# Performance work log

Measured on AMD Instinct MI355X. Metric: run time of the kernel, lower is better.

The kernel has to match this reference:

```python
import jax, jax.numpy as jnp
import numpy as np

H = 1024           # hidden_size
E = 8              # num_experts
I = 4096 // E      # expert_intermediate_size = 512
V = 32000          # vocab_size
T = 4096           # num_tokens


def setup_inputs() -> dict:
    key = jax.random.key(0)
    ks = jax.random.split(key, 6)
    x = jax.random.normal(ks[0], (T, H), dtype=jnp.float32)
    token_ids = jax.random.randint(ks[1], (T,), 0, V, dtype=jnp.int64)
    mu = jax.random.normal(ks[2], (T, H), dtype=jnp.float32)
    # learned parameters (kaiming-like scale)
    gate_up_proj = jax.random.normal(ks[3], (E, H, 2 * I), dtype=jnp.float32) * (1.0 / np.sqrt(H))
    down_proj = jax.random.normal(ks[4], (E, I, H), dtype=jnp.float32) * (1.0 / np.sqrt(I))
    mu_w = jax.random.normal(ks[5], (E, H), dtype=jnp.float32) * 0.02  # mu_router.weight [E, H]
    return {"x": x, "token_ids": token_ids, "mu": mu,
            "gate_up_proj": gate_up_proj, "down_proj": down_proj, "mu_w": mu_w}


def reference(x, token_ids, mu, gate_up_proj, down_proj, mu_w):
    # deterministic base routing: expert = token_id % num_experts
    tid = jnp.clip(token_ids, 0, V - 1)
    base_expert = tid % E                                   # [T]
    # mu router biases the routing decision
    mu_logits = mu @ mu_w.T                                 # [T, E]
    combined = jax.nn.one_hot(base_expert, E, dtype=jnp.float32) * 10.0 + mu_logits
    expert_ids = jnp.argmax(combined, axis=-1)              # [T]

    out = jnp.zeros_like(x)
    # fixed small loop over experts; rows not routed to e are discarded by the mask,
    # so computing the dense GEMM over all tokens gives identical selected rows.
    for e in range(E):
        mask = (expert_ids == e)                            # [T]
        gu = x @ gate_up_proj[e]                            # [T, 2I]
        gate, up = gu[:, :I], gu[:, I:]
        inter = jax.nn.silu(gate) * up                      # [T, I]
        y = inter @ down_proj[e]                            # [T, H]
        out = jnp.where(mask[:, None], y, out)
    return out
```

## Files before the change

### kernel.cpp

```cpp
#include <hip/hip_runtime.h>
#include <cmath>

constexpr int T_DIM = 4096;
constexpr int H_DIM = 1024;
constexpr int E_DIM = 8;
constexpr int I_DIM = 512;
constexpr int V_DIM = 32000;

typedef _Float16 half_t;
typedef __attribute__((ext_vector_type(8))) _Float16 halfx8;
typedef __attribute__((ext_vector_type(4))) _Float16 halfx4;
typedef __attribute__((ext_vector_type(4))) float floatx4;

#define GLOAD16(g, l)                                                        \
    __builtin_amdgcn_global_load_lds(                                        \
        (const __attribute__((address_space(1))) void*)(g),                  \
        (__attribute__((address_space(3))) void*)(l), 16, 0, 0)

constexpr int  CNT_STRIDE  = 16;
constexpr size_t OFF_COUNTS = 0;
constexpr size_t OFF_EID    = 1024;
constexpr size_t OFF_TOKL   = OFF_EID + (size_t)T_DIM * 4;
constexpr size_t OFF_XB     = OFF_TOKL + (size_t)E_DIM * T_DIM * 4;
constexpr size_t OFF_GUPT   = OFF_XB + (size_t)T_DIM * H_DIM * 2;
constexpr size_t OFF_DOWNT  = OFF_GUPT + (size_t)E_DIM * 2 * I_DIM * H_DIM * 2;
constexpr size_t OFF_INTER  = OFF_DOWNT + (size_t)E_DIM * H_DIM * I_DIM * 2;

__global__ __launch_bounds__(256) void prep_kernel(
    const float* __restrict__ x, const float* __restrict__ gup,
    const float* __restrict__ mu, const int* __restrict__ token_ids,
    const float* __restrict__ mu_w, half_t* __restrict__ xb,
    half_t* __restrict__ gupT, int* __restrict__ expert_id)
{
    const int z = blockIdx.z, bx = blockIdx.x, by = blockIdx.y;
    const int tid = threadIdx.x;

    if (z >= 2) {
        const int t = ((z - 2) * 256 + by) * 8 + bx;

        const float4 m = *(const float4*)&mu[(size_t)t * H_DIM + tid * 4];
        float acc[E_DIM];
#pragma unroll
        for (int e = 0; e < E_DIM; ++e) {
            const float4 w = *(const float4*)&mu_w[e * H_DIM + tid * 4];
            acc[e] = m.x * w.x + m.y * w.y + m.z * w.z + m.w * w.w;
        }
#pragma unroll
        for (int e = 0; e < E_DIM; ++e) {
#pragma unroll
            for (int off = 32; off > 0; off >>= 1)
                acc[e] += __shfl_down(acc[e], off, 64);
        }
        __shared__ float part[4][E_DIM];
        const int lane = tid & 63, w = tid >> 6;
        if (lane == 0) {
#pragma unroll
            for (int e = 0; e < E_DIM; ++e) part[w][e] = acc[e];
        }
        __syncthreads();
        if (tid == 0) {
            int tk = token_ids[t];
            tk = min(max(tk, 0), V_DIM - 1);
            const int be = tk & (E_DIM - 1);
            float best = -1e30f; int bi = 0;
#pragma unroll
            for (int e = 0; e < E_DIM; ++e) {
                const float c = part[0][e] + part[1][e] + part[2][e] + part[3][e]
                              + (e == be ? 10.f : 0.f);
                if (c > best) { best = c; bi = e; }
            }
            expert_id[t] = bi;
        }
        return;
    }

    if (z == 1) {
        const int idx = by * 8 + bx;
        if (idx >= 512) return;
#pragma unroll
        for (int p = 0; p < 4; ++p) {
            const size_t i = (size_t)idx * 8192 + p * 2048 + tid * 8;
            const float4 v0 = *(const float4*)&x[i];
            const float4 v1 = *(const float4*)&x[i + 4];
            halfx8 h = { (half_t)v0.x, (half_t)v0.y, (half_t)v0.z, (half_t)v0.w,
                         (half_t)v1.x, (half_t)v1.y, (half_t)v1.z, (half_t)v1.w };
            *(halfx8*)&xb[i] = h;
        }
        return;
    }

    __shared__ float tile[64][65];
    const float* se = gup + (size_t)bx * H_DIM * (2 * I_DIM);
    half_t* de = gupT + (size_t)bx * (2 * I_DIM) * H_DIM;
    constexpr int N = 1024, K = H_DIM;
    const int n0 = (by & 15) * 64, k0 = (by >> 4) * 64;
    const int c4 = (tid & 15) * 4, r0 = tid >> 4;
#pragma unroll
    for (int p = 0; p < 4; ++p) {
        const int r = r0 + p * 16;
        const float4 v = *(const float4*)&se[(size_t)(k0 + r) * N + n0 + c4];
        tile[r][c4 + 0] = v.x; tile[r][c4 + 1] = v.y;
        tile[r][c4 + 2] = v.z; tile[r][c4 + 3] = v.w;
    }
    __syncthreads();
#pragma unroll
    for (int p = 0; p < 4; ++p) {
        const int n = r0 + p * 16;
        const int kc = c4;
        halfx4 h = { (half_t)tile[kc + 0][n], (half_t)tile[kc + 1][n],
                     (half_t)tile[kc + 2][n], (half_t)tile[kc + 3][n] };
        *(halfx4*)&de[(size_t)(n0 + n) * K + k0 + kc] = h;
    }
}

__global__ __launch_bounds__(1024) void scatter_kernel(
    const int* __restrict__ expert_id, int* __restrict__ counts,
    int* __restrict__ tok_list)
{
    const int e = blockIdx.x;
    const int tid = threadIdx.x;
    const int lane = tid & 63, wv = tid >> 6;
    __shared__ int wcnt[16];
    int base = 0;
#pragma unroll
    for (int r = 0; r < 4; ++r) {
        const int t = r * 1024 + tid;
        const bool m = (expert_id[t] == e);
        const unsigned long long mask = __ballot(m);
        const int wrank = (int)__popcll(mask & ((1ull << lane) - 1ull));
        if (lane == 0) wcnt[wv] = (int)__popcll(mask);
        __syncthreads();
        int pre = 0, tot = 0;
#pragma unroll
        for (int i = 0; i < 16; ++i) {
            const int c = wcnt[i];
            pre += (i < wv) ? c : 0;
            tot += c;
        }
        if (m) tok_list[e * T_DIM + base + pre + wrank] = t;
        base += tot;
        __syncthreads();
    }
    if (tid == 0) counts[e * CNT_STRIDE] = base;
}

__global__ __launch_bounds__(256) void gemm1_mfma_kernel(
    const half_t* __restrict__ xb, const half_t* __restrict__ gupT,
    const float* __restrict__ down, half_t* __restrict__ downT,
    const int* __restrict__ counts, const int* __restrict__ tok_list,
    half_t* __restrict__ inter)
{
    __shared__ __align__(16) char smraw[49152 + 64 * 4];
    const int tid = threadIdx.x;
    const int e = blockIdx.x;

    if (blockIdx.z >= 64) {
        float (*tile)[65] = (float (*)[65])smraw;
        const float* se = down + (size_t)e * I_DIM * H_DIM;
        half_t* de = downT + (size_t)e * H_DIM * I_DIM;
        const int n0 = (blockIdx.z - 64) * 64, k0 = blockIdx.y * 64;
        const int c4 = (tid & 15) * 4, r0 = tid >> 4;
#pragma unroll
        for (int p = 0; p < 4; ++p) {
            const int r = r0 + p * 16;
            const float4 v = *(const float4*)&se[(size_t)(k0 + r) * H_DIM + n0 + c4];
            tile[r][c4 + 0] = v.x; tile[r][c4 + 1] = v.y;
            tile[r][c4 + 2] = v.z; tile[r][c4 + 3] = v.w;
        }
        __syncthreads();
#pragma unroll
        for (int p = 0; p < 4; ++p) {
            const int n = r0 + p * 16;
            const int kc = c4;
            halfx4 h = { (half_t)tile[kc + 0][n], (half_t)tile[kc + 1][n],
                         (half_t)tile[kc + 2][n], (half_t)tile[kc + 3][n] };
            *(halfx4*)&de[(size_t)(n0 + n) * I_DIM + k0 + kc] = h;
        }
        return;
    }

    const int count = counts[e * CNT_STRIDE];
    const int m0 = blockIdx.z * 64;
    if (m0 >= count) return;
    const int n0 = blockIdx.y * 64;

    half_t* const As0 = (half_t*)smraw;
    half_t* const As1 = (half_t*)(smraw + 8192);
    half_t* const Bs0 = (half_t*)(smraw + 16384);
    half_t* const Bs1 = (half_t*)(smraw + 32768);
    int* const toks = (int*)(smraw + 49152);

    if (tid < 64) {
        const int m = m0 + tid;
        toks[tid] = (m < count) ? tok_list[e * T_DIM + m] : -1;
    }
    __syncthreads();

    const half_t* We = gupT + (size_t)e * (2 * I_DIM) * H_DIM;

    const int lane = tid & 63;
    const int w = tid >> 6;
    const int lr = lane >> 3, lc = lane & 7;

    const half_t* aptr[2]; const half_t* bptr[4];
    half_t *a0l[2], *a1l[2], *b0l[4], *b1l[4];
#pragma unroll
    for (int j = 0; j < 2; ++j) {
        const int r = w * 16 + j * 8 + lr;
        const int cg = lc ^ (r & 7);
        const int tk = toks[r];
        aptr[j] = xb + (size_t)(tk < 0 ? 0 : tk) * H_DIM + cg * 8;
        const int off = (w * 16 + j * 8) * 64;
        a0l[j] = As0 + off; a1l[j] = As1 + off;
    }
#pragma unroll
    for (int j = 0; j < 4; ++j) {
        const int n = w * 32 + j * 8 + lr;
        const int col = (n < 64) ? (n0 + n) : (I_DIM + n0 + (n - 64));
        const int cg = lc ^ (n & 7);
        bptr[j] = We + (size_t)col * H_DIM + cg * 8;
        const int off = (w * 32 + j * 8) * 64;
        b0l[j] = Bs0 + off; b1l[j] = Bs1 + off;
    }

    const floatx4 fzero = {0.f, 0.f, 0.f, 0.f};
    floatx4 accg[2][2], accu[2][2];
#pragma unroll
    for (int i = 0; i < 2; ++i)
#pragma unroll
        for (int j = 0; j < 2; ++j) { accg[i][j] = fzero; accu[i][j] = fzero; }

    const int wr = w >> 1, wc = w & 1;
    const int fm = lane & 15, q = lane >> 4;
    const int fm7 = fm & 7;

    auto mfma_phase = [&](const half_t* A_, const half_t* B_) {
#pragma unroll
        for (int ks = 0; ks < 2; ++ks) {
            const int swz = ((ks * 4 + q) ^ fm7) * 8;
            const halfx8 a0 = *(const halfx8*)&A_[(32 * wr + fm) * 64 + swz];
            const halfx8 a1 = *(const halfx8*)&A_[(32 * wr + 16 + fm) * 64 + swz];
#pragma unroll
            for (int ct = 0; ct < 2; ++ct) {
                const int ng = wc * 32 + ct * 16 + fm;
                const halfx8 bg = *(const halfx8*)&B_[ng * 64 + swz];
                const halfx8 bu = *(const halfx8*)&B_[(64 + ng) * 64 + swz];
                accg[0][ct] = __builtin_amdgcn_mfma_f32_16x16x32_f16(a0, bg, accg[0][ct], 0, 0, 0);
                accg[1][ct] = __builtin_amdgcn_mfma_f32_16x16x32_f16(a1, bg, accg[1][ct], 0, 0, 0);
                accu[0][ct] = __builtin_amdgcn_mfma_f32_16x16x32_f16(a0, bu, accu[0][ct], 0, 0, 0);
                accu[1][ct] = __builtin_amdgcn_mfma_f32_16x16x32_f16(a1, bu, accu[1][ct], 0, 0, 0);
            }
        }
    };

#pragma unroll
    for (int j = 0; j < 2; ++j) GLOAD16(aptr[j], a0l[j]);
#pragma unroll
    for (int j = 0; j < 4; ++j) GLOAD16(bptr[j], b0l[j]);
    __syncthreads();

    for (int it = 0; it < H_DIM / 64; it += 2) {
        const int k1 = (it + 1) * 64;
        if (k1 < H_DIM) {
#pragma unroll
            for (int j = 0; j < 2; ++j) GLOAD16(aptr[j] + k1, a1l[j]);
#pragma unroll
            for (int j = 0; j < 4; ++j) GLOAD16(bptr[j] + k1, b1l[j]);
        }
        mfma_phase(As0, Bs0);
        __syncthreads();
        const int k2 = (it + 2) * 64;
        if (k2 < H_DIM) {
#pragma unroll
            for (int j = 0; j < 2; ++j) GLOAD16(aptr[j] + k2, a0l[j]);
#pragma unroll
            for (int j = 0; j < 4; ++j) GLOAD16(bptr[j] + k2, b0l[j]);
        }
        mfma_phase(As1, Bs1);
        __syncthreads();
    }

#pragma unroll
    for (int rt = 0; rt < 2; ++rt)
#pragma unroll
        for (int r = 0; r < 4; ++r) {
            const int row = 32 * wr + 16 * rt + q * 4 + r;
            const int tk = toks[row];
            if (tk < 0) continue;
#pragma unroll
            for (int ct = 0; ct < 2; ++ct) {
                const float g = accg[rt][ct][r];
                const float u = accu[rt][ct][r];
                const float s = g / (1.f + __expf(-g)) * u;
                inter[(size_t)tk * I_DIM + n0 + wc * 32 + ct * 16 + fm] = (half_t)s;
            }
        }
}

__global__ __launch_bounds__(256) void gemm2_mfma_kernel(
    const half_t* __restrict__ inter, const half_t* __restrict__ downT,
    const int* __restrict__ counts, const int* __restrict__ tok_list,
    float* __restrict__ out)
{
    const int e = blockIdx.x;
    const int count = counts[e * CNT_STRIDE];
    const int m0 = blockIdx.z * 64;
    if (m0 >= count) return;
    const int n0 = blockIdx.y * 128;

    __shared__ __align__(16) char smraw[49152 + 64 * 4];
    half_t* const As0 = (half_t*)smraw;
    half_t* const As1 = (half_t*)(smraw + 8192);
    half_t* const Bs0 = (half_t*)(smraw + 16384);
    half_t* const Bs1 = (half_t*)(smraw + 32768);
    int* const toks = (int*)(smraw + 49152);

    const int tid = threadIdx.x;
    if (tid < 64) {
        const int m = m0 + tid;
        toks[tid] = (m < count) ? tok_list[e * T_DIM + m] : -1;
    }
    __syncthreads();

    const half_t* De = downT + (size_t)e * H_DIM * I_DIM;

    const int lane = tid & 63;
    const int w = tid >> 6;
    const int lr = lane >> 3, lc = lane & 7;

    const half_t* aptr[2]; const half_t* bptr[4];
    half_t *a0l[2], *a1l[2], *b0l[4], *b1l[4];
#pragma unroll
    for (int j = 0; j < 2; ++j) {
        const int r = w * 16 + j * 8 + lr;
        const int cg = lc ^ (r & 7);
        const int tk = toks[r];
        aptr[j] = inter + (size_t)(tk < 0 ? 0 : tk) * I_DIM + cg * 8;
        const int off = (w * 16 + j * 8) * 64;
        a0l[j] = As0 + off; a1l[j] = As1 + off;
    }
#pragma unroll
    for (int j = 0; j < 4; ++j) {
        const int n = w * 32 + j * 8 + lr;
        const int cg = lc ^ (n & 7);
        bptr[j] = De + (size_t)(n0 + n) * I_DIM + cg * 8;
        const int off = (w * 32 + j * 8) * 64;
        b0l[j] = Bs0 + off; b1l[j] = Bs1 + off;
    }

    const floatx4 fzero = {0.f, 0.f, 0.f, 0.f};
    floatx4 acc[2][4];
#pragma unroll
    for (int i = 0; i < 2; ++i)
#pragma unroll
        for (int j = 0; j < 4; ++j) acc[i][j] = fzero;

    const int wr = w >> 1, wc = w & 1;
    const int fm = lane & 15, q = lane >> 4;
    const int fm7 = fm & 7;

    auto mfma_phase = [&](const half_t* A_, const half_t* B_) {
#pragma unroll
        for (int ks = 0; ks < 2; ++ks) {
            const int swz = ((ks * 4 + q) ^ fm7) * 8;
            const halfx8 a0 = *(const halfx8*)&A_[(32 * wr + fm) * 64 + swz];
            const halfx8 a1 = *(const halfx8*)&A_[(32 * wr + 16 + fm) * 64 + swz];
#pragma unroll
            for (int ct = 0; ct < 4; ++ct) {
                const halfx8 b = *(const halfx8*)&B_[(wc * 64 + ct * 16 + fm) * 64 + swz];
                acc[0][ct] = __builtin_amdgcn_mfma_f32_16x16x32_f16(a0, b, acc[0][ct], 0, 0, 0);
                acc[1][ct] = __builtin_amdgcn_mfma_f32_16x16x32_f16(a1, b, acc[1][ct], 0, 0, 0);
            }
        }
    };

#pragma unroll
    for (int j = 0; j < 2; ++j) GLOAD16(aptr[j], a0l[j]);
#pragma unroll
    for (int j = 0; j < 4; ++j) GLOAD16(bptr[j], b0l[j]);
    __syncthreads();

    for (int it = 0; it < I_DIM / 64; it += 2) {
        const int k1 = (it + 1) * 64;
        if (k1 < I_DIM) {
#pragma unroll
            for (int j = 0; j < 2; ++j) GLOAD16(aptr[j] + k1, a1l[j]);
#pragma unroll
            for (int j = 0; j < 4; ++j) GLOAD16(bptr[j] + k1, b1l[j]);
        }
        mfma_phase(As0, Bs0);
        __syncthreads();
        const int k2 = (it + 2) * 64;
        if (k2 < I_DIM) {
#pragma unroll
            for (int j = 0; j < 2; ++j) GLOAD16(aptr[j] + k2, a0l[j]);
#pragma unroll
            for (int j = 0; j < 4; ++j) GLOAD16(bptr[j] + k2, b0l[j]);
        }
        mfma_phase(As1, Bs1);
        __syncthreads();
    }

#pragma unroll
    for (int rt = 0; rt < 2; ++rt)
#pragma unroll
        for (int r = 0; r < 4; ++r) {
            const int row = 32 * wr + 16 * rt + q * 4 + r;
            const int tk = toks[row];
            if (tk < 0) continue;
#pragma unroll
            for (int ct = 0; ct < 4; ++ct)
                out[(size_t)tk * H_DIM + n0 + wc * 64 + ct * 16 + fm] = acc[rt][ct][r];
        }
}

extern "C" void kernel_launch(void* const* d_in, const int* in_sizes, int n_in,
                              void* d_out, int out_size, void* d_ws, size_t ws_size,
                              hipStream_t stream)
{
    const float* x         = (const float*)d_in[0];
    const int*   token_ids = (const int*)  d_in[1];
    const float* mu        = (const float*)d_in[2];
    const float* gup       = (const float*)d_in[3];
    const float* down      = (const float*)d_in[4];
    const float* mu_w      = (const float*)d_in[5];
    float* out = (float*)d_out;

    char* ws = (char*)d_ws;
    int*    counts    = (int*)(ws + OFF_COUNTS);
    int*    expert_id = (int*)(ws + OFF_EID);
    int*    tok_list  = (int*)(ws + OFF_TOKL);
    half_t* xb        = (half_t*)(ws + OFF_XB);
    half_t* gupT      = (half_t*)(ws + OFF_GUPT);
    half_t* downT     = (half_t*)(ws + OFF_DOWNT);
    half_t* inter     = (half_t*)(ws + OFF_INTER);

    prep_kernel<<<dim3(8, 256, 4), 256, 0, stream>>>(
        x, gup, mu, token_ids, mu_w, xb, gupT, expert_id);
    scatter_kernel<<<E_DIM, 1024, 0, stream>>>(expert_id, counts, tok_list);
    gemm1_mfma_kernel<<<dim3(E_DIM, 8, 80), 256, 0, stream>>>(
        xb, gupT, down, downT, counts, tok_list, inter);
    gemm2_mfma_kernel<<<dim3(E_DIM, 8, T_DIM / 64), 256, 0, stream>>>(
        inter, downT, counts, tok_list, out);
}
```

Before: 156.7 us.

## Fuse all four stages into one persistent cooperative kernel with grid syncs

Replaces the four separate launches (routing prep, scatter, gemm1 plus down transpose, gemm2) with a single cooperative kernel of 512 persistent blocks. Work is distributed with grid-stride loops and separated by grid.sync barriers. This removes the launch gaps between kernels. In exchange it serialises stages that previously overlapped (routing vs weight transposes), adds grid barrier cost, and caps concurrency at 512 blocks for the GEMMs.

Result: slower. 338.9 us (+116.2%).

```diff
diff --git a/kernel.cpp b/kernel.cpp
--- a/kernel.cpp
+++ b/kernel.cpp
@@ -1,5 +1,8 @@
 #include <hip/hip_runtime.h>
+#include <hip/hip_cooperative_groups.h>
 #include <cmath>
+
+namespace cg = cooperative_groups;
 
 constexpr int T_DIM = 4096;
 constexpr int H_DIM = 1024;
@@ -26,163 +29,152 @@
 constexpr size_t OFF_DOWNT  = OFF_GUPT + (size_t)E_DIM * 2 * I_DIM * H_DIM * 2;
 constexpr size_t OFF_INTER  = OFF_DOWNT + (size_t)E_DIM * H_DIM * I_DIM * 2;
 
-__global__ __launch_bounds__(256) void prep_kernel(
+__global__ __launch_bounds__(256) void fused_kernel(
     const float* __restrict__ x, const float* __restrict__ gup,
-    const float* __restrict__ mu, const int* __restrict__ token_ids,
-    const float* __restrict__ mu_w, half_t* __restrict__ xb,
-    half_t* __restrict__ gupT, int* __restrict__ expert_id)
+    const float* __restrict__ down, const float* __restrict__ mu,
+    const int* __restrict__ token_ids, const float* __restrict__ mu_w,
+    half_t* __restrict__ xb, half_t* __restrict__ gupT,
+    half_t* __restrict__ downT, int* __restrict__ expert_id,
+    int* __restrict__ counts, int* __restrict__ tok_list,
+    half_t* __restrict__ inter, float* __restrict__ out)
 {
-    const int z = blockIdx.z, bx = blockIdx.x, by = blockIdx.y;
+    __shared__ __align__(16) char smraw[49152 + 256];
     const int tid = threadIdx.x;
-
-    if (z >= 2) {
-        const int t = ((z - 2) * 256 + by) * 8 + bx;
-
-        const float4 m = *(const float4*)&mu[(size_t)t * H_DIM + tid * 4];
-        float acc[E_DIM];
-#pragma unroll
-        for (int e = 0; e < E_DIM; ++e) {
-            const float4 w = *(const float4*)&mu_w[e * H_DIM + tid * 4];
-            acc[e] = m.x * w.x + m.y * w.y + m.z * w.z + m.w * w.w;
-        }
-#pragma unroll
-        for (int e = 0; e < E_DIM; ++e) {
-#pragma unroll
-            for (int off = 32; off > 0; off >>= 1)
-                acc[e] += __shfl_down(acc[e], off, 64);
-        }
-        __shared__ float part[4][E_DIM];
-        const int lane = tid & 63, w = tid >> 6;
-        if (lane == 0) {
-#pragma unroll
-            for (int e = 0; e < E_DIM; ++e) part[w][e] = acc[e];
-        }
-        __syncthreads();
-        if (tid == 0) {
-            int tk = token_ids[t];
-            tk = min(max(tk, 0), V_DIM - 1);
-            const int be = tk & (E_DIM - 1);
-            float best = -1e30f; int bi = 0;
+    const int bx = blockIdx.x;
+    const int NB = gridDim.x;
+    const int lane = tid & 63, wv = tid >> 6;
+    cg::grid_group grid = cg::this_grid();
+
+    {
+        float (*part)[E_DIM] = (float (*)[E_DIM])smraw;
+        for (int t = bx; t < T_DIM; t += NB) {
+            const float4 m = *(const float4*)&mu[(size_t)t * H_DIM + tid * 4];
+            float acc[E_DIM];
 #pragma unroll
             for (int e = 0; e < E_DIM; ++e) {
-                const float c = part[0][e] + part[1][e] + part[2][e] + part[3][e]
-                              + (e == be ? 10.f : 0.f);
-                if (c > best) { best = c; bi = e; }
-            }
-            expert_id[t] = bi;
-        }
-        return;
+                const float4 w = *(const float4*)&mu_w[e * H_DIM + tid * 4];
+                acc[e] = m.x * w.x + m.y * w.y + m.z * w.z + m.w * w.w;
+            }
+#pragma unroll
+            for (int e = 0; e < E_DIM; ++e) {
+#pragma unroll
+                for (int off = 32; off > 0; off >>= 1)
+                    acc[e] += __shfl_down(acc[e], off, 64);
+            }
+            if (lane == 0) {
+#pragma unroll
+                for (int e = 0; e < E_DIM; ++e) part[wv][e] = acc[e];
+            }
+            __syncthreads();
+            if (tid == 0) {
+                int tk = token_ids[t];
+                tk = min(max(tk, 0), V_DIM - 1);
+                const int be = tk & (E_DIM - 1);
+                float best = -1e30f; int bi = 0;
+#pragma unroll
+                for (int e = 0; e < E_DIM; ++e) {
+                    const float c = part[0][e] + part[1][e] + part[2][e] + part[3][e]
+                                  + (e == be ? 10.f : 0.f);
+                    if (c > best) { best = c; bi = e; }
+                }
+                expert_id[t] = bi;
+            }
+            __syncthreads();
+        }
     }
-
-    if (z == 1) {
-        const int idx = by * 8 + bx;
-        if (idx >= 512) return;
-#pragma unroll
-        for (int p = 0; p < 4; ++p) {
-            const size_t i = (size_t)idx * 8192 + p * 2048 + tid * 8;
-            const float4 v0 = *(const float4*)&x[i];
-            const float4 v1 = *(const float4*)&x[i + 4];
-            halfx8 h = { (half_t)v0.x, (half_t)v0.y, (half_t)v0.z, (half_t)v0.w,
-                         (half_t)v1.x, (half_t)v1.y, (half_t)v1.z, (half_t)v1.w };
-            *(halfx8*)&xb[i] = h;
-        }
-        return;
+    grid.sync();
+
+    {
+        constexpr int N_SC = 8, N_GT = 2048, N_CV = 512, N_DT = 1024;
+        for (int it = bx; it < N_SC + N_GT + N_CV + N_DT; it += NB) {
+            if (it < N_SC) {
+                const int e = it;
+                int* wcnt = (int*)smraw;
+                int base = 0;
+#pragma unroll 1
+                for (int r = 0; r < 16; ++r) {
+                    const int t = r * 256 + tid;
+                    const bool m = (expert_id[t] == e);
+                    const unsigned long long mask = __ballot(m);
+                    const int wrank = (int)__popcll(mask & ((1ull << lane) - 1ull));
+                    if (lane == 0) wcnt[wv] = (int)__popcll(mask);
+                    __syncthreads();
+                    int pre = 0, tot = 0;
+#pragma unroll
+                    for (int i = 0; i < 4; ++i) {
+                        const int c = wcnt[i];
+                        pre += (i < wv) ? c : 0;
+                        tot += c;
+                    }
+                    if (m) tok_list[e * T_DIM + base + pre + wrank] = t;
+                    base += tot;
+                    __syncthreads();
+                }
+                if (tid == 0) counts[e * CNT_STRIDE] = base;
+                __syncthreads();
+            } else if (it < N_SC + N_GT) {
+                const int tno = it - N_SC;
+                const int e = tno >> 8, r = tno & 255;
+                const int n0 = (r & 15) * 64, k0 = (r >> 4) * 64;
+                float (*tile)[65] = (float (*)[65])smraw;
+                const float* se = gup + (size_t)e * H_DIM * (2 * I_DIM);
+                half_t* de = gupT + (size_t)e * (2 * I_DIM) * H_DIM;
+                const int c4 = (tid & 15) * 4, r0 = tid >> 4;
+#pragma unroll
+                for (int p = 0; p < 4; ++p) {
+                    const int rr = r0 + p * 16;
+                    const float4 v = *(const float4*)&se[(size_t)(k0 + rr) * 1024 + n0 + c4];
+                    tile[rr][c4 + 0] = v.x; tile[rr][c4 + 1] = v.y;
+                    tile[rr][c4 + 2] = v.z; tile[rr][c4 + 3] = v.w;
+                }
+                __syncthreads();
+#pragma unroll
+                for (int p = 0; p < 4; ++p) {
+                    const int n = r0 + p * 16;
+                    halfx4 h = { (half_t)tile[c4 + 0][n], (half_t)tile[c4 + 1][n],
+                                 (half_t)tile[c4 + 2][n], (half_t)tile[c4 + 3][n] };
+                    *(halfx4*)&de[(size_t)(n0 + n) * H_DIM + k0 + c4] = h;
+                }
+                __syncthreads();
+            } else if (it < N_SC + N_GT + N_CV) {
+                const int idx = it - (N_SC + N_GT);
+#pragma unroll
+                for (int p = 0; p < 4; ++p) {
+                    const size_t i = (size_t)idx * 8192 + p * 2048 + tid * 8;
+                    const float4 v0 = *(const float4*)&x[i];
+                    const float4 v1 = *(const float4*)&x[i + 4];
+                    halfx8 h = { (half_t)v0.x, (half_t)v0.y, (half_t)v0.z, (half_t)v0.w,
+                                 (half_t)v1.x, (half_t)v1.y, (half_t)v1.z, (half_t)v1.w };
+                    *(halfx8*)&xb[i] = h;
+                }
+            } else {
+                const int tno = it - (N_SC + N_GT + N_CV);
+                const int e = tno >> 7, r = tno & 127;
+                const int n0 = (r & 15) * 64, k0 = (r >> 4) * 64;
+                float (*tile)[65] = (float (*)[65])smraw;
+                const float* se = down + (size_t)e * I_DIM * H_DIM;
+                half_t* de = downT + (size_t)e * H_DIM * I_DIM;
+                const int c4 = (tid & 15) * 4, r0 = tid >> 4;
+#pragma unroll
+                for (int p = 0; p < 4; ++p) {
+                    const int rr = r0 + p * 16;
+                    const float4 v = *(const float4*)&se[(size_t)(k0 + rr) * H_DIM + n0 + c4];
+                    tile[rr][c4 + 0] = v.x; tile[rr][c4 + 1] = v.y;
+                    tile[rr][c4 + 2] = v.z; tile[rr][c4 + 3] = v.w;
+                }
+                __syncthreads();
+#pragma unroll
+                for (int p = 0; p < 4; ++p) {
+                    const int n = r0 + p * 16;
+                    halfx4 h = { (half_t)tile[c4 + 0][n], (half_t)tile[c4 + 1][n],
+                                 (half_t)tile[c4 + 2][n], (half_t)tile[c4 + 3][n] };
+                    *(halfx4*)&de[(size_t)(n0 + n) * I_DIM + k0 + c4] = h;
+                }
+                __syncthreads();
+            }
+        }
     }
-
-    __shared__ float tile[64][65];
-    const float* se = gup + (size_t)bx * H_DIM * (2 * I_DIM);
-    half_t* de = gupT + (size_t)bx * (2 * I_DIM) * H_DIM;
-    constexpr int N = 1024, K = H_DIM;
-    const int n0 = (by & 15) * 64, k0 = (by >> 4) * 64;
-    const int c4 = (tid & 15) * 4, r0 = tid >> 4;
-#pragma unroll
-    for (int p = 0; p < 4; ++p) {
-        const int r = r0 + p * 16;
-        const float4 v = *(const float4*)&se[(size_t)(k0 + r) * N + n0 + c4];
-        tile[r][c4 + 0] = v.x; tile[r][c4 + 1] = v.y;
-        tile[r][c4 + 2] = v.z; tile[r][c4 + 3] = v.w;
-    }
-    __syncthreads();
-#pragma unroll
-    for (int p = 0; p < 4; ++p) {
-        const int n = r0 + p * 16;
-        const int kc = c4;
-        halfx4 h = { (half_t)tile[kc + 0][n], (half_t)tile[kc + 1][n],
-                     (half_t)tile[kc + 2][n], (half_t)tile[kc + 3][n] };
-        *(halfx4*)&de[(size_t)(n0 + n) * K + k0 + kc] = h;
-    }
-}
-
-__global__ __launch_bounds__(1024) void scatter_kernel(
-    const int* __restrict__ expert_id, int* __restrict__ counts,
-    int* __restrict__ tok_list)
-{
-    const int e = blockIdx.x;
-    const int tid = threadIdx.x;
-    const int lane = tid & 63, wv = tid >> 6;
-    __shared__ int wcnt[16];
-    int base = 0;
-#pragma unroll
-    for (int r = 0; r < 4; ++r) {
-        const int t = r * 1024 + tid;
-        const bool m = (expert_id[t] == e);
-        const unsigned long long mask = __ballot(m);
-        const int wrank = (int)__popcll(mask & ((1ull << lane) - 1ull));
-        if (lane == 0) wcnt[wv] = (int)__popcll(mask);
-        __syncthreads();
-        int pre = 0, tot = 0;
-#pragma unroll
-        for (int i = 0; i < 16; ++i) {
-            const int c = wcnt[i];
-            pre += (i < wv) ? c : 0;
-            tot += c;
-        }
-        if (m) tok_list[e * T_DIM + base + pre + wrank] = t;
-        base += tot;
-        __syncthreads();
-    }
-    if (tid == 0) counts[e * CNT_STRIDE] = base;
-}
-
-__global__ __launch_bounds__(256) void gemm1_mfma_kernel(
-    const half_t* __restrict__ xb, const half_t* __restrict__ gupT,
-    const float* __restrict__ down, half_t* __restrict__ downT,
-    const int* __restrict__ counts, const int* __restrict__ tok_list,
-    half_t* __restrict__ inter)
-{
-    __shared__ __align__(16) char smraw[49152 + 64 * 4];
-    const int tid = threadIdx.x;
-    const int e = blockIdx.x;
-
-    if (blockIdx.z >= 64) {
-        float (*tile)[65] = (float (*)[65])smraw;
-        const float* se = down + (size_t)e * I_DIM * H_DIM;
-        half_t* de = downT + (size_t)e * H_DIM * I_DIM;
-        const int n0 = (blockIdx.z - 64) * 64, k0 = blockIdx.y * 64;
-        const int c4 = (tid & 15) * 4, r0 = tid >> 4;
-#pragma unroll
-        for (int p = 0; p < 4; ++p) {
-            const int r = r0 + p * 16;
-            const float4 v = *(const float4*)&se[(size_t)(k0 + r) * H_DIM + n0 + c4];
-            tile[r][c4 + 0] = v.x; tile[r][c4 + 1] = v.y;
-            tile[r][c4 + 2] = v.z; tile[r][c4 + 3] = v.w;
-        }
-        __syncthreads();
-#pragma unroll
-        for (int p = 0; p < 4; ++p) {
-            const int n = r0 + p * 16;
-            const int kc = c4;
-            halfx4 h = { (half_t)tile[kc + 0][n], (half_t)tile[kc + 1][n],
-                         (half_t)tile[kc + 2][n], (half_t)tile[kc + 3][n] };
-            *(halfx4*)&de[(size_t)(n0 + n) * I_DIM + k0 + kc] = h;
-        }
-        return;
-    }
-
-    const int count = counts[e * CNT_STRIDE];
-    const int m0 = blockIdx.z * 64;
-    if (m0 >= count) return;
-    const int n0 = blockIdx.y * 64;
+    grid.sync();
 
     half_t* const As0 = (half_t*)smraw;
     half_t* const As1 = (half_t*)(smraw + 8192);
@@ -190,228 +182,218 @@
     half_t* const Bs1 = (half_t*)(smraw + 32768);
     int* const toks = (int*)(smraw + 49152);
 
-    if (tid < 64) {
-        const int m = m0 + tid;
-        toks[tid] = (m < count) ? tok_list[e * T_DIM + m] : -1;
-    }
-    __syncthreads();
-
-    const half_t* We = gupT + (size_t)e * (2 * I_DIM) * H_DIM;
-
-    const int lane = tid & 63;
     const int w = tid >> 6;
     const int lr = lane >> 3, lc = lane & 7;
-
-    const half_t* aptr[2]; const half_t* bptr[4];
-    half_t *a0l[2], *a1l[2], *b0l[4], *b1l[4];
-#pragma unroll
-    for (int j = 0; j < 2; ++j) {
-        const int r = w * 16 + j * 8 + lr;
-        const int cg = lc ^ (r & 7);
-        const int tk = toks[r];
-        aptr[j] = xb + (size_t)(tk < 0 ? 0 : tk) * H_DIM + cg * 8;
-        const int off = (w * 16 + j * 8) * 64;
-        a0l[j] = As0 + off; a1l[j] = As1 + off;
-    }
-#pragma unroll
-    for (int j = 0; j < 4; ++j) {
-        const int n = w * 32 + j * 8 + lr;
-        const int col = (n < 64) ? (n0 + n) : (I_DIM + n0 + (n - 64));
-        const int cg = lc ^ (n & 7);
-        bptr[j] = We + (size_t)col * H_DIM + cg * 8;
-        const int off = (w * 32 + j * 8) * 64;
-        b0l[j] = Bs0 + off; b1l[j] = Bs1 + off;
-    }
-
-    const floatx4 fzero = {0.f, 0.f, 0.f, 0.f};
-    floatx4 accg[2][2], accu[2][2];
-#pragma unroll
-    for (int i = 0; i < 2; ++i)
-#pragma unroll
-        for (int j = 0; j < 2; ++j) { accg[i][j] = fzero; accu[i][j] = fzero; }
-
     const int wr = w >> 1, wc = w & 1;
     const int fm = lane & 15, q = lane >> 4;
     const int fm7 = fm & 7;
-
-    auto mfma_phase = [&](const half_t* A_, const half_t* B_) {
-#pragma unroll
-        for (int ks = 0; ks < 2; ++ks) {
-            const int swz = ((ks * 4 + q) ^ fm7) * 8;
-            const halfx8 a0 = *(const halfx8*)&A_[(32 * wr + fm) * 64 + swz];
-            const halfx8 a1 = *(const halfx8*)&A_[(32 * wr + 16 + fm) * 64 + swz];
-#pragma unroll
-            for (int ct = 0; ct < 2; ++ct) {
-                const int ng = wc * 32 + ct * 16 + fm;
-                const halfx8 bg = *(const halfx8*)&B_[ng * 64 + swz];
-                const halfx8 bu = *(const halfx8*)&B_[(64 + ng) * 64 + swz];
-                accg[0][ct] = __builtin_amdgcn_mfma_f32_16x16x32_f16(a0, bg, accg[0][ct], 0, 0, 0);
-                accg[1][ct] = __builtin_amdgcn_mfma_f32_16x16x32_f16(a1, bg, accg[1][ct], 0, 0, 0);
-                accu[0][ct] = __builtin_amdgcn_mfma_f32_16x16x32_f16(a0, bu, accu[0][ct], 0, 0, 0);
-                accu[1][ct] = __builtin_amdgcn_mfma_f32_16x16x32_f16(a1, bu, accu[1][ct], 0, 0, 0);
-            }
-        }
-    };
-
-#pragma unroll
-    for (int j = 0; j < 2; ++j) GLOAD16(aptr[j], a0l[j]);
-#pragma unroll
-    for (int j = 0; j < 4; ++j) GLOAD16(bptr[j], b0l[j]);
-    __syncthreads();
-
-    for (int it = 0; it < H_DIM / 64; it += 2) {
-        const int k1 = (it + 1) * 64;
-        if (k1 < H_DIM) {
-#pragma unroll
-            for (int j = 0; j < 2; ++j) GLOAD16(aptr[j] + k1, a1l[j]);
-#pragma unroll
-            for (int j = 0; j < 4; ++j) GLOAD16(bptr[j] + k1, b1l[j]);
-        }
-        mfma_phase(As0, Bs0);
-        __syncthreads();
-        const int k2 = (it + 2) * 64;
-        if (k2 < H_DIM) {
-#pragma unroll
-            for (int j = 0; j < 2; ++j) GLOAD16(aptr[j] + k2, a0l[j]);
-#pragma unroll
-            for (int j = 0; j < 4; ++j) GLOAD16(bptr[j] + k2, b0l[j]);
-        }
-        mfma_phase(As1, Bs1);
+    const floatx4 fzero = {0.f, 0.f, 0.f, 0.f};
+
+    for (int it = bx; it < E_DIM * 8 * 64; it += NB) {
+        const int e = it & 7;
+        const int rest = it >> 3;
+        const int n0 = (rest & 7) * 64;
+        const int m0 = (rest >> 3) * 64;
+        const int count = counts[e * CNT_STRIDE];
+        if (m0 >= count) continue;
+
+        if (tid < 64) {
+            const int m = m0 + tid;
+            toks[tid] = (m < count) ? tok_list[e * T_DIM + m] : -1;
+        }
+        __syncthreads();
+
+        const half_t* We = gupT + (size_t)e * (2 * I_DIM) * H_DIM;
+
+        const half_t* aptr[2]; const half_t* bptr[4];
+        half_t *a0l[2], *a1l[2], *b0l[4], *b1l[4];
+#pragma unroll
+        for (int j = 0; j < 2; ++j) {
+            const int r = w * 16 + j * 8 + lr;
+            const int cg_ = lc ^ (r & 7);
+            const int tk = toks[r];
+            aptr[j] = xb + (size_t)(tk < 0 ? 0 : tk) * H_DIM + cg_ * 8;
+            const int off = (w * 16 + j * 8) * 64;
+            a0l[j] = As0 + off; a1l[j] = As1 + off;
+        }
+#pragma unroll
+        for (int j = 0; j < 4; ++j) {
+            const int n = w * 32 + j * 8 + lr;
+            const int col = (n < 64) ? (n0 + n) : (I_DIM + n0 + (n - 64));
+            const int cg_ = lc ^ (n & 7);
+            bptr[j] = We + (size_t)col * H_DIM + cg_ * 8;
+            const int off = (w * 32 + j * 8) * 64;
+            b0l[j] = Bs0 + off; b1l[j] = Bs1 + off;
+        }
+
+        floatx4 accg[2][2], accu[2][2];
+#pragma unroll
+        for (int i = 0; i < 2; ++i)
+#pragma unroll
+            for (int j = 0; j < 2; ++j) { accg[i][j] = fzero; accu[i][j] = fzero; }
+
+        auto mfma_phase = [&](const half_t* A_, const half_t* B_) {
+#pragma unroll
+            for (int ks = 0; ks < 2; ++ks) {
+                const int swz = ((ks * 4 + q) ^ fm7) * 8;
+                const halfx8 a0 = *(const halfx8*)&A_[(32 * wr + fm) * 64 + swz];
+                const halfx8 a1 = *(const halfx8*)&A_[(32 * wr + 16 + fm) * 64 + swz];
+#pragma unroll
+                for (int ct = 0; ct < 2; ++ct) {
+                    const int ng = wc * 32 + ct * 16 + fm;
+                    const halfx8 bg = *(const halfx8*)&B_[ng * 64 + swz];
+                    const halfx8 bu = *(const halfx8*)&B_[(64 + ng) * 64 + swz];
+                    accg[0][ct] = __builtin_amdgcn_mfma_f32_16x16x32_f16(a0, bg, accg[0][ct], 0, 0, 0);
+                    accg[1][ct] = __builtin_amdgcn_mfma_f32_16x16x32_f16(a1, bg, accg[1][ct], 0, 0, 0);
+                    accu[0][ct] = __builtin_amdgcn_mfma_f32_16x16x32_f16(a0, bu, accu[0][ct], 0, 0, 0);
+                    accu[1][ct] = __builtin_amdgcn_mfma_f32_16x16x32_f16(a1, bu, accu[1][ct], 0, 0, 0);
+                }
+            }
+        };
+
+#pragma unroll
+        for (int j = 0; j < 2; ++j) GLOAD16(aptr[j], a0l[j]);
+#pragma unroll
+        for (int j = 0; j < 4; ++j) GLOAD16(bptr[j], b0l[j]);
+        __syncthreads();
+
+        for (int kit = 0; kit < H_DIM / 64; kit += 2) {
+            const int k1 = (kit + 1) * 64;
+            if (k1 < H_DIM) {
+#pragma unroll
+                for (int j = 0; j < 2; ++j) GLOAD16(aptr[j] + k1, a1l[j]);
+#pragma unroll
+                for (int j = 0; j < 4; ++j) GLOAD16(bptr[j] + k1, b1l[j]);
+            }
+            mfma_phase(As0, Bs0);
+            __syncthreads();
+            const int k2 = (kit + 2) * 64;
+            if (k2 < H_DIM) {
+#pragma unroll
+                for (int j = 0; j < 2; ++j) GLOAD16(aptr[j] + k2, a0l[j]);
+#pragma unroll
+                for (int j = 0; j < 4; ++j) GLOAD16(bptr[j] + k2, b0l[j]);
+            }
+            mfma_phase(As1, Bs1);
+            __syncthreads();
+        }
+
+#pragma unroll
+        for (int rt = 0; rt < 2; ++rt)
+#pragma unroll
+            for (int r = 0; r < 4; ++r) {
+                const int row = 32 * wr + 16 * rt + q * 4 + r;
+                const int tk = toks[row];
+                if (tk < 0) continue;
+#pragma unroll
+                for (int ct = 0; ct < 2; ++ct) {
+                    const float g = accg[rt][ct][r];
+                    const float u = accu[rt][ct][r];
+                    const float s = g / (1.f + __expf(-g)) * u;
+                    inter[(size_t)tk * I_DIM + n0 + wc * 32 + ct * 16 + fm] = (half_t)s;
+                }
+            }
         __syncthreads();
     }
-
-#pragma unroll
-    for (int rt = 0; rt < 2; ++rt)
-#pragma unroll
-        for (int r = 0; r < 4; ++r) {
-            const int row = 32 * wr + 16 * rt + q * 4 + r;
-            const int tk = toks[row];
-            if (tk < 0) continue;
-#pragma unroll
-            for (int ct = 0; ct < 2; ++ct) {
-                const float g = accg[rt][ct][r];
-                const float u = accu[rt][ct][r];
-                const float s = g / (1.f + __expf(-g)) * u;
-                inter[(size_t)tk * I_DIM + n0 + wc * 32 + ct * 16 + fm] = (half_t)s;
-            }
-        }
-}
-
-__global__ __launch_bounds__(256) void gemm2_mfma_kernel(
-    const half_t* __restrict__ inter, const half_t* __restrict__ downT,
-    const int* __restrict__ counts, const int* __restrict__ tok_list,
-    float* __restrict__ out)
-{
-    const int e = blockIdx.x;
-    const int count = counts[e * CNT_STRIDE];
-    const int m0 = blockIdx.z * 64;
-    if (m0 >= count) return;
-    const int n0 = blockIdx.y * 128;
-
-    __shared__ __align__(16) char smraw[49152 + 64 * 4];
-    half_t* const As0 = (half_t*)smraw;
-    half_t* const As1 = (half_t*)(smraw + 8192);
-    half_t* const Bs0 = (half_t*)(smraw + 16384);
-    half_t* const Bs1 = (half_t*)(smraw + 32768);
-    int* const toks = (int*)(smraw + 49152);
-
-    const int tid = threadIdx.x;
-    if (tid < 64) {
-        const int m = m0 + tid;
-        toks[tid] = (m < count) ? tok_list[e * T_DIM + m] : -1;
+    grid.sync();
+
+    for (int it = bx; it < E_DIM * 8 * 64; it += NB) {
+        const int e = it & 7;
+        const int rest = it >> 3;
+        const int n0 = (rest & 7) * 128;
+        const int m0 = (rest >> 3) * 64;
+        const int count = counts[e * CNT_STRIDE];
+        if (m0 >= count) continue;
+
+        if (tid < 64) {
+            const int m = m0 + tid;
+            toks[tid] = (m < count) ? tok_list[e * T_DIM + m] : -1;
+        }
+        __syncthreads();
+
+        const half_t* De = downT + (size_t)e * H_DIM * I_DIM;
+
+        const half_t* aptr[2]; const half_t* bptr[4];
+        half_t *a0l[2], *a1l[2], *b0l[4], *b1l[4];
+#pragma unroll
+        for (int j = 0; j < 2; ++j) {
+            const int r = w * 16 + j * 8 + lr;
+            const int cg_ = lc ^ (r & 7);
+            const int tk = toks[r];
+            aptr[j] = inter + (size_t)(tk < 0 ? 0 : tk) * I_DIM + cg_ * 8;
+            const int off = (w * 16 + j * 8) * 64;
+            a0l[j] = As0 + off; a1l[j] = As1 + off;
+        }
+#pragma unroll
+        for (int j = 0; j < 4; ++j) {
+            const int n = w * 32 + j * 8 + lr;
+            const int cg_ = lc ^ (n & 7);
+            bptr[j] = De + (size_t)(n0 + n) * I_DIM + cg_ * 8;
+            const int off = (w * 32 + j * 8) * 64;
+            b0l[j] = Bs0 + off; b1l[j] = Bs1 + off;
+        }
+
+        floatx4 acc[2][4];
+#pragma unroll
+        for (int i = 0; i < 2; ++i)
+#pragma unroll
+            for (int j = 0; j < 4; ++j) acc[i][j] = fzero;
+
+        auto mfma_phase2 = [&](const half_t* A_, const half_t* B_) {
+#pragma unroll
+            for (int ks = 0; ks < 2; ++ks) {
+                const int swz = ((ks * 4 + q) ^ fm7) * 8;
+                const halfx8 a0 = *(const halfx8*)&A_[(32 * wr + fm) * 64 + swz];
+                const halfx8 a1 = *(const halfx8*)&A_[(32 * wr + 16 + fm) * 64 + swz];
+#pragma unroll
+                for (int ct = 0; ct < 4; ++ct) {
+                    const halfx8 b = *(const halfx8*)&B_[(wc * 64 + ct * 16 + fm) * 64 + swz];
+                    acc[0][ct] = __builtin_amdgcn_mfma_f32_16x16x32_f16(a0, b, acc[0][ct], 0, 0, 0);
+                    acc[1][ct] = __builtin_amdgcn_mfma_f32_16x16x32_f16(a1, b, acc[1][ct], 0, 0, 0);
+                }
+            }
+        };
+
+#pragma unroll
+        for (int j = 0; j < 2; ++j) GLOAD16(aptr[j], a0l[j]);
+#pragma unroll
+        for (int j = 0; j < 4; ++j) GLOAD16(bptr[j], b0l[j]);
+        __syncthreads();
+
+        for (int kit = 0; kit < I_DIM / 64; kit += 2) {
+            const int k1 = (kit + 1) * 64;
+            if (k1 < I_DIM) {
+#pragma unroll
+                for (int j = 0; j < 2; ++j) GLOAD16(aptr[j] + k1, a1l[j]);
+#pragma unroll
+                for (int j = 0; j < 4; ++j) GLOAD16(bptr[j] + k1, b1l[j]);
+            }
+            mfma_phase2(As0, Bs0);
+            __syncthreads();
+            const int k2 = (kit + 2) * 64;
+            if (k2 < I_DIM) {
+#pragma unroll
+                for (int j = 0; j < 2; ++j) GLOAD16(aptr[j] + k2, a0l[j]);
+#pragma unroll
+                for (int j = 0; j < 4; ++j) GLOAD16(bptr[j] + k2, b0l[j]);
+            }
+            mfma_phase2(As1, Bs1);
+            __syncthreads();
+        }
+
+#pragma unroll
+        for (int rt = 0; rt < 2; ++rt)
+#pragma unroll
+            for (int r = 0; r < 4; ++r) {
+                const int row = 32 * wr + 16 * rt + q * 4 + r;
+                const int tk = toks[row];
+                if (tk < 0) continue;
+#pragma unroll
+                for (int ct = 0; ct < 4; ++ct)
+                    out[(size_t)tk * H_DIM + n0 + wc * 64 + ct * 16 + fm] = acc[rt][ct][r];
+            }
+        __syncthreads();
     }
-    __syncthreads();
-
-    const half_t* De = downT + (size_t)e * H_DIM * I_DIM;
-
-    const int lane = tid & 63;
-    const int w = tid >> 6;
-    const int lr = lane >> 3, lc = lane & 7;
-
-    const half_t* aptr[2]; const half_t* bptr[4];
-    half_t *a0l[2], *a1l[2], *b0l[4], *b1l[4];
-#pragma unroll
-    for (int j = 0; j < 2; ++j) {
-        const int r = w * 16 + j * 8 + lr;
-        const int cg = lc ^ (r & 7);
-        const int tk = toks[r];
-        aptr[j] = inter + (size_t)(tk < 0 ? 0 : tk) * I_DIM + cg * 8;
-        const int off = (w * 16 + j * 8) * 64;
-        a0l[j] = As0 + off; a1l[j] = As1 + off;
-    }
-#pragma unroll
-    for (int j = 0; j < 4; ++j) {
-        const int n = w * 32 + j * 8 + lr;
-        const int cg = lc ^ (n & 7);
-        bptr[j] = De + (size_t)(n0 + n) * I_DIM + cg * 8;
-        const int off = (w * 32 + j * 8) * 64;
-        b0l[j] = Bs0 + off; b1l[j] = Bs1 + off;
-    }
-
-    const floatx4 fzero = {0.f, 0.f, 0.f, 0.f};
-    floatx4 acc[2][4];
-#pragma unroll
-    for (int i = 0; i < 2; ++i)
-#pragma unroll
-        for (int j = 0; j < 4; ++j) acc[i][j] = fzero;
-
-    const int wr = w >> 1, wc = w & 1;
-    const int fm = lane & 15, q = lane >> 4;
-    const int fm7 = fm & 7;
-
-    auto mfma_phase = [&](const half_t* A_, const half_t* B_) {
-#pragma unroll
-        for (int ks = 0; ks < 2; ++ks) {
-            const int swz = ((ks * 4 + q) ^ fm7) * 8;
-            const halfx8 a0 = *(const halfx8*)&A_[(32 * wr + fm) * 64 + swz];
-            const halfx8 a1 = *(const halfx8*)&A_[(32 * wr + 16 + fm) * 64 + swz];
-#pragma unroll
-            for (int ct = 0; ct < 4; ++ct) {
-                const halfx8 b = *(const halfx8*)&B_[(wc * 64 + ct * 16 + fm) * 64 + swz];
-                acc[0][ct] = __builtin_amdgcn_mfma_f32_16x16x32_f16(a0, b, acc[0][ct], 0, 0, 0);
-                acc[1][ct] = __builtin_amdgcn_mfma_f32_16x16x32_f16(a1, b, acc[1][ct], 0, 0, 0);
-            }
-        }
-    };
-
-#pragma unroll
-    for (int j = 0; j < 2; ++j) GLOAD16(aptr[j], a0l[j]);
-#pragma unroll
-    for (int j = 0; j < 4; ++j) GLOAD16(bptr[j], b0l[j]);
-    __syncthreads();
-
-    for (int it = 0; it < I_DIM / 64; it += 2) {
-        const int k1 = (it + 1) * 64;
-        if (k1 < I_DIM) {
-#pragma unroll
-            for (int j = 0; j < 2; ++j) GLOAD16(aptr[j] + k1, a1l[j]);
-#pragma unroll
-            for (int j = 0; j < 4; ++j) GLOAD16(bptr[j] + k1, b1l[j]);
-        }
-        mfma_phase(As0, Bs0);
-        __syncthreads();
-        const int k2 = (it + 2) * 64;
-        if (k2 < I_DIM) {
-#pragma unroll
-            for (int j = 0; j < 2; ++j) GLOAD16(aptr[j] + k2, a0l[j]);
-#pragma unroll
-            for (int j = 0; j < 4; ++j) GLOAD16(bptr[j] + k2, b0l[j]);
-        }
-        mfma_phase(As1, Bs1);
-        __syncthreads();
-    }
-
-#pragma unroll
-    for (int rt = 0; rt < 2; ++rt)
-#pragma unroll
-        for (int r = 0; r < 4; ++r) {
-            const int row = 32 * wr + 16 * rt + q * 4 + r;
-            const int tk = toks[row];
-            if (tk < 0) continue;
-#pragma unroll
-            for (int ct = 0; ct < 4; ++ct)
-                out[(size_t)tk * H_DIM + n0 + wc * 64 + ct * 16 + fm] = acc[rt][ct][r];
-        }
 }
 
 extern "C" void kernel_launch(void* const* d_in, const int* in_sizes, int n_in,
@@ -435,11 +417,12 @@
     half_t* downT     = (half_t*)(ws + OFF_DOWNT);
     half_t* inter     = (half_t*)(ws + OFF_INTER);
 
-    prep_kernel<<<dim3(8, 256, 4), 256, 0, stream>>>(
-        x, gup, mu, token_ids, mu_w, xb, gupT, expert_id);
-    scatter_kernel<<<E_DIM, 1024, 0, stream>>>(expert_id, counts, tok_list);
-    gemm1_mfma_kernel<<<dim3(E_DIM, 8, 80), 256, 0, stream>>>(
-        xb, gupT, down, downT, counts, tok_list, inter);
-    gemm2_mfma_kernel<<<dim3(E_DIM, 8, T_DIM / 64), 256, 0, stream>>>(
-        inter, downT, counts, tok_list, out);
+    void* kargs[] = {
+        (void*)&x, (void*)&gup, (void*)&down, (void*)&mu,
+        (void*)&token_ids, (void*)&mu_w,
+        (void*)&xb, (void*)&gupT, (void*)&downT, (void*)&expert_id,
+        (void*)&counts, (void*)&tok_list, (void*)&inter, (void*)&out
+    };
+    hipLaunchCooperativeKernel((const void*)fused_kernel,
+                               dim3(512), dim3(256), kargs, 0, stream);
 }
```

## Deepen LDS double-buffer prefetch with explicit vmcnt waits and raw barriers

Applied to the files above, without the earlier changes.

Both expert GEMM kernels now issue loads for the first two K-tiles before the loop and keep one tile in flight at all times. Each iteration waits only for the older tile's global-to-LDS loads (vmcnt(6)) rather than draining every outstanding load with __syncthreads. The loop is fully unrolled, and sched_barrier plus s_setprio are added around the MFMA phase so waves are prioritised while computing. The goal is more overlap between global loads and MFMA. The cost is reliance on hand-counted vmcnt values and compiler scheduling fences, which could break correctness if the number of outstanding loads per thread changes.

New measurement: 156.5 us. No clear change (-0.1%).

```diff
diff --git a/kernel.cpp b/kernel.cpp
--- a/kernel.cpp
+++ b/kernel.cpp
@@ -257,27 +257,40 @@
     for (int j = 0; j < 2; ++j) GLOAD16(aptr[j], a0l[j]);
 #pragma unroll
     for (int j = 0; j < 4; ++j) GLOAD16(bptr[j], b0l[j]);
-    __syncthreads();
-
-    for (int it = 0; it < H_DIM / 64; it += 2) {
-        const int k1 = (it + 1) * 64;
-        if (k1 < H_DIM) {
-#pragma unroll
-            for (int j = 0; j < 2; ++j) GLOAD16(aptr[j] + k1, a1l[j]);
-#pragma unroll
-            for (int j = 0; j < 4; ++j) GLOAD16(bptr[j] + k1, b1l[j]);
-        }
-        mfma_phase(As0, Bs0);
-        __syncthreads();
+#pragma unroll
+    for (int j = 0; j < 2; ++j) GLOAD16(aptr[j] + 64, a1l[j]);
+#pragma unroll
+    for (int j = 0; j < 4; ++j) GLOAD16(bptr[j] + 64, b1l[j]);
+
+    constexpr int NSTEP1 = H_DIM / 64;
+#pragma unroll
+    for (int it = 0; it < NSTEP1; ++it) {
+        if (it < NSTEP1 - 1) asm volatile("s_waitcnt vmcnt(6)" ::: "memory");
+        else                 asm volatile("s_waitcnt vmcnt(0)" ::: "memory");
+        __builtin_amdgcn_s_barrier();
+        __builtin_amdgcn_sched_barrier(0);
+        __builtin_amdgcn_s_setprio(1);
+        if ((it & 1) == 0) mfma_phase(As0, Bs0);
+        else               mfma_phase(As1, Bs1);
+        __builtin_amdgcn_s_setprio(0);
+        asm volatile("s_waitcnt lgkmcnt(0)" ::: "memory");
+        __builtin_amdgcn_sched_barrier(0);
+        __builtin_amdgcn_s_barrier();
+        __builtin_amdgcn_sched_barrier(0);
         const int k2 = (it + 2) * 64;
         if (k2 < H_DIM) {
-#pragma unroll
-            for (int j = 0; j < 2; ++j) GLOAD16(aptr[j] + k2, a0l[j]);
-#pragma unroll
-            for (int j = 0; j < 4; ++j) GLOAD16(bptr[j] + k2, b0l[j]);
-        }
-        mfma_phase(As1, Bs1);
-        __syncthreads();
+            if ((it & 1) == 0) {
+#pragma unroll
+                for (int j = 0; j < 2; ++j) GLOAD16(aptr[j] + k2, a0l[j]);
+#pragma unroll
+                for (int j = 0; j < 4; ++j) GLOAD16(bptr[j] + k2, b0l[j]);
+            } else {
+#pragma unroll
+                for (int j = 0; j < 2; ++j) GLOAD16(aptr[j] + k2, a1l[j]);
+#pragma unroll
+                for (int j = 0; j < 4; ++j) GLOAD16(bptr[j] + k2, b1l[j]);
+            }
+        }
     }
 
 #pragma unroll
@@ -378,27 +391,40 @@
     for (int j = 0; j < 2; ++j) GLOAD16(aptr[j], a0l[j]);
 #pragma unroll
     for (int j = 0; j < 4; ++j) GLOAD16(bptr[j], b0l[j]);
-    __syncthreads();
-
-    for (int it = 0; it < I_DIM / 64; it += 2) {
-        const int k1 = (it + 1) * 64;
-        if (k1 < I_DIM) {
-#pragma unroll
-            for (int j = 0; j < 2; ++j) GLOAD16(aptr[j] + k1, a1l[j]);
-#pragma unroll
-            for (int j = 0; j < 4; ++j) GLOAD16(bptr[j] + k1, b1l[j]);
-        }
-        mfma_phase(As0, Bs0);
-        __syncthreads();
+#pragma unroll
+    for (int j = 0; j < 2; ++j) GLOAD16(aptr[j] + 64, a1l[j]);
+#pragma unroll
+    for (int j = 0; j < 4; ++j) GLOAD16(bptr[j] + 64, b1l[j]);
+
+    constexpr int NSTEP2 = I_DIM / 64;
+#pragma unroll
+    for (int it = 0; it < NSTEP2; ++it) {
+        if (it < NSTEP2 - 1) asm volatile("s_waitcnt vmcnt(6)" ::: "memory");
+        else                 asm volatile("s_waitcnt vmcnt(0)" ::: "memory");
+        __builtin_amdgcn_s_barrier();
+        __builtin_amdgcn_sched_barrier(0);
+        __builtin_amdgcn_s_setprio(1);
+        if ((it & 1) == 0) mfma_phase(As0, Bs0);
+        else               mfma_phase(As1, Bs1);
+        __builtin_amdgcn_s_setprio(0);
+        asm volatile("s_waitcnt lgkmcnt(0)" ::: "memory");
+        __builtin_amdgcn_sched_barrier(0);
+        __builtin_amdgcn_s_barrier();
+        __builtin_amdgcn_sched_barrier(0);
         const int k2 = (it + 2) * 64;
         if (k2 < I_DIM) {
-#pragma unroll
-            for (int j = 0; j < 2; ++j) GLOAD16(aptr[j] + k2, a0l[j]);
-#pragma unroll
-            for (int j = 0; j < 4; ++j) GLOAD16(bptr[j] + k2, b0l[j]);
-        }
-        mfma_phase(As1, Bs1);
-        __syncthreads();
+            if ((it & 1) == 0) {
+#pragma unroll
+                for (int j = 0; j < 2; ++j) GLOAD16(aptr[j] + k2, a0l[j]);
+#pragma unroll
+                for (int j = 0; j < 4; ++j) GLOAD16(bptr[j] + k2, b0l[j]);
+            } else {
+#pragma unroll
+                for (int j = 0; j < 2; ++j) GLOAD16(aptr[j] + k2, a1l[j]);
+#pragma unroll
+                for (int j = 0; j < 4; ++j) GLOAD16(bptr[j] + k2, b1l[j]);
+            }
+        }
     }
 
 #pragma unroll
```
